# Performance work log

Measured on AMD Instinct MI355X. Metric: run time of the kernel, lower is better.

The kernel has to match this reference:

```python
import jax, jax.numpy as jnp
import numpy as np

NEG_SLOPE = 0.2  # PyG GATConv default negative_slope


def gat_conv(x, W, a_src, a_dst, bias, src, dst, heads, out_c, concat):
    """PyG-style GATConv with self-loops. x:[N,F_in], W:[F_in,heads*out_c]."""
    N = x.shape[0]
    # add self loops
    loop = jnp.arange(N, dtype=src.dtype)
    src = jnp.concatenate([src, loop])
    dst = jnp.concatenate([dst, loop])
    h = (x @ W).reshape(N, heads, out_c)            # [N,H,C]
    alpha_src = jnp.sum(h * a_src, axis=-1)          # [N,H]
    alpha_dst = jnp.sum(h * a_dst, axis=-1)          # [N,H]
    e = jax.nn.leaky_relu(alpha_src[src] + alpha_dst[dst], NEG_SLOPE)  # [E,H]
    # segment softmax over incoming edges of each destination node
    m = jax.ops.segment_max(e, dst, num_segments=N)  # [N,H]
    ex = jnp.exp(e - m[dst])
    s = jax.ops.segment_sum(ex, dst, num_segments=N)
    alpha = ex / (s[dst] + 1e-16)                    # [E,H]
    msg = h[src] * alpha[:, :, None]                 # [E,H,C]
    out = jax.ops.segment_sum(msg, dst, num_segments=N)  # [N,H,C]
    out = out.reshape(N, heads * out_c) if concat else out.mean(axis=1)
    return out + bias


def setup_inputs() -> dict:
    key = jax.random.key(0)
    ks = jax.random.split(key, 16)
    N, E = 25000, 400000
    node_dim, hidden, out_dim, heads = 64, 128, 256, 4

    def glorot(k, shape):
        fan = shape[0] + shape[-1]
        return jax.random.normal(k, shape, jnp.float32) * np.sqrt(2.0 / fan)

    return {
        "x": jax.random.normal(ks[0], (N, node_dim), jnp.float32),
        "edge_index": jax.random.randint(ks[1], (2, E), 0, N, jnp.int32),
        "W_emb": glorot(ks[2], (node_dim, hidden)),
        "b_emb": jnp.zeros((hidden,), jnp.float32),
        "W1": glorot(ks[3], (hidden, heads * hidden)),
        "a1_src": glorot(ks[4], (heads, hidden)),
        "a1_dst": glorot(ks[5], (heads, hidden)),
        "b1": jnp.zeros((heads * hidden,), jnp.float32),
        "W2": glorot(ks[6], (heads * hidden, hidden)),
        "a2_src": glorot(ks[7], (1, hidden)),
        "a2_dst": glorot(ks[8], (1, hidden)),
        "b2": jnp.zeros((hidden,), jnp.float32),
        "W_out": glorot(ks[9], (hidden, out_dim)),
        "b_out": jnp.zeros((out_dim,), jnp.float32),
    }


def reference(x, edge_index, W_emb, b_emb, W1, a1_src, a1_dst, b1, W2, a2_src, a2_dst, b2, W_out, b_out):
    src, dst = edge_index[0], edge_index[1]
    heads, hidden = a1_src.shape[0], a1_src.shape[1]
    h = jax.nn.relu(x @ W_emb + b_emb)                 # dropout is identity in eval
    h = gat_conv(h, W1, a1_src, a1_dst, b1, src, dst, heads, hidden, True)
    h = jax.nn.elu(h)
    h = gat_conv(h, W2, a2_src, a2_dst, b2, src, dst, 1, hidden, False)
    h = jax.nn.elu(h)
    g = jnp.mean(h, axis=0, keepdims=True)             # global mean pool, batch=None -> [1, hidden]
    return g @ W_out + b_out                           # [1, out_dim]
```

## Files before the change

### kernel.cpp

```cpp
#include <hip/hip_runtime.h>
#include <hip/hip_bf16.h>


#define LRELU(x) ((x) > 0.f ? (x) : 0.2f * (x))

typedef short bf16x8 __attribute__((ext_vector_type(8)));
typedef float f32x4 __attribute__((ext_vector_type(4)));
typedef float f32x2 __attribute__((ext_vector_type(2)));

static __device__ __forceinline__ unsigned short f2b(float f) {
    union { float f; unsigned u; } x; x.f = f;
    unsigned r = x.u + 0x7fff + ((x.u >> 16) & 1);
    return (unsigned short)(r >> 16);
}
static __device__ __forceinline__ float rl_f(float v, int c) {
    return __int_as_float(__builtin_amdgcn_readlane(__float_as_int(v), c));
}
static __device__ __forceinline__ unsigned char f2fp8(float v) {
    int p = __builtin_amdgcn_cvt_pk_fp8_f32(v, v, 0, false);
    return (unsigned char)(p & 0xff);
}

__global__ void zero_kernel(int* __restrict__ deg, float* __restrict__ pool,
                            int* __restrict__ done, int* __restrict__ flg,
                            int* __restrict__ agg, int N, int nb) {
    int i = blockIdx.x * blockDim.x + threadIdx.x;
    if (i < N) { deg[i] = 0; return; }
    i -= N;
    if (i < 128) { pool[i] = 0.f; return; }
    i -= 128;
    if (i == 0) { *done = 0; return; }
    i -= 1;
    if (i < nb) { flg[i] = 0; return; }
    i -= nb;
    if (i < nb) agg[i] = 0;
}

__global__ void degcount_prep(const int* __restrict__ ei, int E, int N,
                              int* __restrict__ deg, int blocksE,
                              const float* __restrict__ x, const float* __restrict__ We,
                              const float* __restrict__ W1, const float* __restrict__ W2,
                              unsigned short* __restrict__ xb, unsigned short* __restrict__ WeT,
                              unsigned short* __restrict__ W1T, unsigned short* __restrict__ W2T,
                              int Nx) {
    if ((int)blockIdx.x < blocksE) {
        int i = blockIdx.x * blockDim.x + threadIdx.x;
        if (i < E) atomicAdd(&deg[ei[E + i]], 1);
        else if (i < E + N) atomicAdd(&deg[i - E], 1);
        return;
    }
    int i = (blockIdx.x - blocksE) * blockDim.x + threadIdx.x;
    if (i < Nx) { xb[i] = f2b(x[i]); return; }
    i -= Nx;
    if (i < 64 * 128) { int k = i >> 7, n = i & 127; WeT[n * 64 + k] = f2b(We[i]); return; }
    i -= 64 * 128;
    if (i < 128 * 512) { int k = i >> 9, n = i & 511; W1T[n * 128 + k] = f2b(W1[i]); return; }
    i -= 128 * 512;
    if (i < 512 * 128) { int k = i >> 7, n = i & 127; W2T[n * 512 + k] = f2b(W2[i]); return; }
}

__global__ __launch_bounds__(256) void scan_lookback(const int* __restrict__ deg,
                                                     int* __restrict__ rowptr,
                                                     int* __restrict__ cursor,
                                                     int* __restrict__ agg,
                                                     int* __restrict__ flg,
                                                     int N, int nb) {
    __shared__ int sd[256];
    __shared__ int soff;
    int t = threadIdx.x, b = blockIdx.x;
    int i = b * 256 + t;
    int d = (i < N) ? deg[i] : 0;
    sd[t] = d;
    __syncthreads();
    for (int off = 1; off < 256; off <<= 1) {
        int v = (t >= off) ? sd[t - off] : 0;
        __syncthreads();
        sd[t] += v;
        __syncthreads();
    }
    int incl = sd[t];
    int btot = sd[255];
    if (t == 0) {
        soff = 0;
        __hip_atomic_store(&agg[b], btot, __ATOMIC_RELAXED, __HIP_MEMORY_SCOPE_AGENT);
        __hip_atomic_store(&flg[b], 1, __ATOMIC_RELEASE, __HIP_MEMORY_SCOPE_AGENT);
    }
    if (b > 0 && t < 64) {
        int acc = 0;
        for (int p = t; p < b; p += 64) {
            while (__hip_atomic_load(&flg[p], __ATOMIC_ACQUIRE, __HIP_MEMORY_SCOPE_AGENT) == 0)
                __builtin_amdgcn_s_sleep(1);
            acc += __hip_atomic_load(&agg[p], __ATOMIC_RELAXED, __HIP_MEMORY_SCOPE_AGENT);
        }
#pragma unroll
        for (int o = 32; o >= 1; o >>= 1) acc += __shfl_xor(acc, o);
        if (t == 0) soff = acc;
    }
    __syncthreads();
    int off = soff;
    int excl = off + incl - d;
    if (i < N) { rowptr[i] = excl; cursor[i] = excl; }
    if (b == nb - 1 && t == 255) rowptr[N] = off + btot;
}

__global__ __launch_bounds__(256) void scatter_gemm12(const int* __restrict__ ei, int E, int Nn,
                                                      int* __restrict__ cursor, int* __restrict__ esrc,
                                                      int blocksE,
                                                      const unsigned short* __restrict__ A,
                                                      const unsigned short* __restrict__ WeT,
                                                      const float* __restrict__ b_emb,
                                                      const unsigned short* __restrict__ W1T,
                                                      unsigned char* __restrict__ C8,
                                                      const float* __restrict__ a_src,
                                                      const float* __restrict__ a_dst,
                                                      float* __restrict__ as_out,
                                                      float* __restrict__ ad_out, int M) {
    __shared__ __align__(16) unsigned short smem[22016];
    __shared__ float sAl[128][2];

    if ((int)blockIdx.x < blocksE) {
        int i = blockIdx.x * 256 + threadIdx.x;
        int s, d;
        if (i < E) { s = ei[i]; d = ei[E + i]; }
        else if (i < E + Nn) { s = i - E; d = s; }
        else return;
        int pos = atomicAdd(&cursor[d], 1);
        esrc[pos] = s;
        return;
    }

    unsigned short* Asx = smem;
    unsigned short* Bwe = smem + 9216;
    unsigned short* h0s = smem;
    unsigned short* Bs  = smem + 16896;

    int g = blockIdx.x - blocksE;
    int bx = g & 3, by = g >> 2;
    int tid = threadIdx.x;
    int gm0 = by * 128, gn0 = bx * 128;
    int w = tid >> 6, lane = tid & 63;
    int wrow = (w >> 1) * 64, wcol = (w & 1) * 64;
    int l15 = lane & 15, quad = lane >> 4;

    f32x4 acc[4][4];
#pragma unroll
    for (int i = 0; i < 4; i++)
#pragma unroll
        for (int j = 0; j < 4; j++) acc[i][j] = {0.f, 0.f, 0.f, 0.f};

#pragma unroll
    for (int rr = 0; rr < 4; rr++) {
        int lin = tid + rr * 256;
        int row = lin >> 3;
        int cg = (lin & 7) * 8;
        int grow = gm0 + row; if (grow >= M) grow = M - 1;
        *(uint4*)&Asx[row * 72 + cg] = *(const uint4*)&A[(size_t)grow * 64 + cg];
        *(uint4*)&Bwe[row * 72 + cg] = *(const uint4*)&WeT[(size_t)row * 64 + cg];
    }
    __syncthreads();
#pragma unroll
    for (int k0 = 0; k0 < 64; k0 += 32) {
        bf16x8 af[4], bfr[4];
#pragma unroll
        for (int i = 0; i < 4; i++) {
            af[i]  = *(const bf16x8*)&Asx[(wrow + i * 16 + l15) * 72 + k0 + quad * 8];
            bfr[i] = *(const bf16x8*)&Bwe[(wcol + i * 16 + l15) * 72 + k0 + quad * 8];
        }
#pragma unroll
        for (int i = 0; i < 4; i++)
#pragma unroll
            for (int j = 0; j < 4; j++)
                acc[i][j] = __builtin_amdgcn_mfma_f32_16x16x32_bf16(af[i], bfr[j], acc[i][j], 0, 0, 0);
    }
    __syncthreads();

#pragma unroll
    for (int j = 0; j < 4; j++) {
        int col = wcol + j * 16 + l15;
        float bv = b_emb[col];
#pragma unroll
        for (int i = 0; i < 4; i++) {
            int row = wrow + i * 16 + quad * 4;
#pragma unroll
            for (int r = 0; r < 4; r++) {
                float v = fmaxf(acc[i][j][r] + bv, 0.f);
                h0s[(row + r) * 132 + col] = f2b(v);
            }
        }
    }

#pragma unroll
    for (int i = 0; i < 4; i++)
#pragma unroll
        for (int j = 0; j < 4; j++) acc[i][j] = {0.f, 0.f, 0.f, 0.f};

    for (int k0 = 0; k0 < 128; k0 += 32) {
#pragma unroll
        for (int rr = 0; rr < 2; rr++) {
            int lin = tid + rr * 256;
            int row = lin >> 2;
            int cg = (lin & 3) * 8;
            *(uint4*)&Bs[row * 40 + cg] = *(const uint4*)&W1T[(size_t)(gn0 + row) * 128 + k0 + cg];
        }
        __syncthreads();
        bf16x8 af[4], bfr[4];
#pragma unroll
        for (int i = 0; i < 4; i++) {
            af[i]  = *(const bf16x8*)&h0s[(wrow + i * 16 + l15) * 132 + k0 + quad * 8];
            bfr[i] = *(const bf16x8*)&Bs[(wcol + i * 16 + l15) * 40 + quad * 8];
        }
#pragma unroll
        for (int i = 0; i < 4; i++)
#pragma unroll
            for (int j = 0; j < 4; j++)
                acc[i][j] = __builtin_amdgcn_mfma_f32_16x16x32_bf16(af[i], bfr[j], acc[i][j], 0, 0, 0);
        __syncthreads();
    }

#pragma unroll
    for (int i = 0; i < 4; i++) {
        int row = gm0 + wrow + i * 16 + quad * 4;
#pragma unroll
        for (int j = 0; j < 4; j++) {
            int col = gn0 + wcol + j * 16 + l15;
#pragma unroll
            for (int r = 0; r < 4; r++) {
                int gr = row + r;
                if (gr < M) C8[(size_t)gr * 512 + col] = f2fp8(acc[i][j][r]);
            }
        }
    }

    {
        int hh = bx;
        float as_c[4], ad_c[4];
#pragma unroll
        for (int j = 0; j < 4; j++) {
            int c = gn0 + wcol + j * 16 + l15;
            as_c[j] = a_src[c];
            ad_c[j] = a_dst[c];
        }
#pragma unroll
        for (int i = 0; i < 4; i++) {
#pragma unroll
            for (int r = 0; r < 4; r++) {
                float ps = 0.f, pd = 0.f;
#pragma unroll
                for (int j = 0; j < 4; j++) {
                    ps += acc[i][j][r] * as_c[j];
                    pd += acc[i][j][r] * ad_c[j];
                }
#pragma unroll
                for (int o = 1; o < 16; o <<= 1) {
                    ps += __shfl_xor(ps, o);
                    pd += __shfl_xor(pd, o);
                }
                if (wcol == 64 && l15 == 0) {
                    int lr = wrow + i * 16 + quad * 4 + r;
                    sAl[lr][0] = ps;
                    sAl[lr][1] = pd;
                }
            }
        }
        __syncthreads();
        if (wcol == 0) {
#pragma unroll
            for (int i = 0; i < 4; i++) {
#pragma unroll
                for (int r = 0; r < 4; r++) {
                    float ps = 0.f, pd = 0.f;
#pragma unroll
                    for (int j = 0; j < 4; j++) {
                        ps += acc[i][j][r] * as_c[j];
                        pd += acc[i][j][r] * ad_c[j];
                    }
#pragma unroll
                    for (int o = 1; o < 16; o <<= 1) {
                        ps += __shfl_xor(ps, o);
                        pd += __shfl_xor(pd, o);
                    }
                    if (l15 == 0) {
                        int lr = wrow + i * 16 + quad * 4 + r;
                        int gr = gm0 + lr;
                        if (gr < M) {
                            as_out[(size_t)gr * 4 + hh] = ps + sAl[lr][0];
                            ad_out[(size_t)gr * 4 + hh] = pd + sAl[lr][1];
                        }
                    }
                }
            }
        }
    }
}

template <int ACT, int OFMT, int ALPHA, int H>
__global__ __launch_bounds__(256) void gemm_mfma_nt(const unsigned short* __restrict__ A,
                                                    const unsigned short* __restrict__ Bt,
                                                    const float* __restrict__ bias,
                                                    void* __restrict__ Cout,
                                                    const float* __restrict__ a_src,
                                                    const float* __restrict__ a_dst,
                                                    float* __restrict__ as_out,
                                                    float* __restrict__ ad_out,
                                                    int M, int N, int K) {
    __shared__ __align__(16) unsigned short As[128 * 40];
    __shared__ __align__(16) unsigned short Bs[128 * 40];
    __shared__ float sAl[128][2];
    int tid = threadIdx.x;
    int gm0 = blockIdx.y * 128, gn0 = blockIdx.x * 128;
    int w = tid >> 6, lane = tid & 63;
    int wrow = (w >> 1) * 64, wcol = (w & 1) * 64;
    int l15 = lane & 15, quad = lane >> 4;

    f32x4 acc[4][4];
#pragma unroll
    for (int i = 0; i < 4; i++)
#pragma unroll
        for (int j = 0; j < 4; j++) acc[i][j] = {0.f, 0.f, 0.f, 0.f};

    for (int k0 = 0; k0 < K; k0 += 32) {
#pragma unroll
        for (int rr = 0; rr < 2; rr++) {
            int lin = tid + rr * 256;
            int row = lin >> 2;
            int cg = (lin & 3) * 8;
            int grow = gm0 + row; if (grow >= M) grow = M - 1;
            uint4 va = *(const uint4*)&A[(size_t)grow * K + k0 + cg];
            *(uint4*)&As[row * 40 + cg] = va;
            uint4 vb = *(const uint4*)&Bt[(size_t)(gn0 + row) * K + k0 + cg];
            *(uint4*)&Bs[row * 40 + cg] = vb;
        }
        __syncthreads();
        bf16x8 af[4], bfr[4];
#pragma unroll
        for (int i = 0; i < 4; i++) {
            af[i]  = *(const bf16x8*)&As[(wrow + i * 16 + l15) * 40 + quad * 8];
            bfr[i] = *(const bf16x8*)&Bs[(wcol + i * 16 + l15) * 40 + quad * 8];
        }
#pragma unroll
        for (int i = 0; i < 4; i++)
#pragma unroll
            for (int j = 0; j < 4; j++)
                acc[i][j] = __builtin_amdgcn_mfma_f32_16x16x32_bf16(af[i], bfr[j], acc[i][j], 0, 0, 0);
        __syncthreads();
    }

    if (OFMT == 0) {
        unsigned short* C = (unsigned short*)Cout;
#pragma unroll
        for (int i = 0; i < 4; i++) {
            int row = gm0 + wrow + i * 16 + quad * 4;
#pragma unroll
            for (int j = 0; j < 4; j++) {
                int col = gn0 + wcol + j * 16 + l15;
                float bv = bias ? bias[col] : 0.f;
#pragma unroll
                for (int r = 0; r < 4; r++) {
                    int gr = row + r;
                    if (gr < M) {
                        float v = acc[i][j][r] + bv;
                        if (ACT == 1) v = fmaxf(v, 0.f);
                        C[(size_t)gr * N + col] = f2b(v);
                    }
                }
            }
        }
    } else {
        unsigned char* C8 = (unsigned char*)Cout;
#pragma unroll
        for (int i = 0; i < 4; i++) {
            int row = gm0 + wrow + i * 16 + quad * 4;
#pragma unroll
            for (int j = 0; j < 4; j++) {
                int col = gn0 + wcol + j * 16 + l15;
#pragma unroll
                for (int r = 0; r < 4; r++) {
                    int gr = row + r;
                    if (gr < M) C8[(size_t)gr * N + col] = f2fp8(acc[i][j][r]);
                }
            }
        }
    }

    if (ALPHA) {
        int hh = blockIdx.x;
        float as_c[4], ad_c[4];
#pragma unroll
        for (int j = 0; j < 4; j++) {
            int c = gn0 + wcol + j * 16 + l15;
            as_c[j] = a_src[c];
            ad_c[j] = a_dst[c];
        }
#pragma unroll
        for (int i = 0; i < 4; i++) {
#pragma unroll
            for (int r = 0; r < 4; r++) {
                float ps = 0.f, pd = 0.f;
#pragma unroll
                for (int j = 0; j < 4; j++) {
                    ps += acc[i][j][r] * as_c[j];
                    pd += acc[i][j][r] * ad_c[j];
                }
#pragma unroll
                for (int o = 1; o < 16; o <<= 1) {
                    ps += __shfl_xor(ps, o);
                    pd += __shfl_xor(pd, o);
                }
                if (wcol == 64 && l15 == 0) {
                    int lr = wrow + i * 16 + quad * 4 + r;
                    sAl[lr][0] = ps;
                    sAl[lr][1] = pd;
                }
            }
        }
        __syncthreads();
        if (wcol == 0) {
#pragma unroll
            for (int i = 0; i < 4; i++) {
#pragma unroll
                for (int r = 0; r < 4; r++) {
                    float ps = 0.f, pd = 0.f;
#pragma unroll
                    for (int j = 0; j < 4; j++) {
                        ps += acc[i][j][r] * as_c[j];
                        pd += acc[i][j][r] * ad_c[j];
                    }
#pragma unroll
                    for (int o = 1; o < 16; o <<= 1) {
                        ps += __shfl_xor(ps, o);
                        pd += __shfl_xor(pd, o);
                    }
                    if (l15 == 0) {
                        int lr = wrow + i * 16 + quad * 4 + r;
                        int gr = gm0 + lr;
                        if (gr < M) {
                            as_out[(size_t)gr * H + hh] = ps + sAl[lr][0];
                            ad_out[(size_t)gr * H + hh] = pd + sAl[lr][1];
                        }
                    }
                }
            }
        }
    }
}

__global__ __launch_bounds__(256) void gat_agg_l1(const unsigned* __restrict__ hq,
                                                  const float4* __restrict__ as4,
                                                  const float4* __restrict__ ad4,
                                                  const int* __restrict__ rowptr,
                                                  const int* __restrict__ esrc,
                                                  const float* __restrict__ bias,
                                                  unsigned short* __restrict__ out, int N) {
    __shared__ float wlds_all[4][256];
    int w = threadIdx.x >> 6, lane = threadIdx.x & 63;
    int n = blockIdx.x * 4 + w;
    if (n >= N) return;
    float* wlds = wlds_all[w];
    int2 rp = *(const int2*)&rowptr[n];
    int begin = rp.x, deg = rp.y - rp.x;
    float4 adn = ad4[n];

    int s_l0 = 0;
    float4 e0 = {-3.4e38f, -3.4e38f, -3.4e38f, -3.4e38f};
    if (lane < deg) {
        s_l0 = esrc[begin + lane];
        float4 u = as4[s_l0];
        e0.x = LRELU(u.x + adn.x); e0.y = LRELU(u.y + adn.y);
        e0.z = LRELU(u.z + adn.z); e0.w = LRELU(u.w + adn.w);
    }
    float4 m = e0;
    for (int base = 64; base < deg; base += 64) {
        int j = base + lane;
        if (j < deg) {
            float4 u = as4[esrc[begin + j]];
            m.x = fmaxf(m.x, LRELU(u.x + adn.x)); m.y = fmaxf(m.y, LRELU(u.y + adn.y));
            m.z = fmaxf(m.z, LRELU(u.z + adn.z)); m.w = fmaxf(m.w, LRELU(u.w + adn.w));
        }
    }
#pragma unroll
    for (int o = 32; o >= 1; o >>= 1) {
        m.x = fmaxf(m.x, __shfl_xor(m.x, o));
        m.y = fmaxf(m.y, __shfl_xor(m.y, o));
        m.z = fmaxf(m.z, __shfl_xor(m.z, o));
        m.w = fmaxf(m.w, __shfl_xor(m.w, o));
    }
    float4 s4 = {0.f, 0.f, 0.f, 0.f};
    if (lane < deg) {
        s4.x = __expf(e0.x - m.x); s4.y = __expf(e0.y - m.y);
        s4.z = __expf(e0.z - m.z); s4.w = __expf(e0.w - m.w);
    }
    for (int base = 64; base < deg; base += 64) {
        int j = base + lane;
        if (j < deg) {
            float4 u = as4[esrc[begin + j]];
            s4.x += __expf(LRELU(u.x + adn.x) - m.x); s4.y += __expf(LRELU(u.y + adn.y) - m.y);
            s4.z += __expf(LRELU(u.z + adn.z) - m.z); s4.w += __expf(LRELU(u.w + adn.w) - m.w);
        }
    }
#pragma unroll
    for (int o = 32; o >= 1; o >>= 1) {
        s4.x += __shfl_xor(s4.x, o); s4.y += __shfl_xor(s4.y, o);
        s4.z += __shfl_xor(s4.z, o); s4.w += __shfl_xor(s4.w, o);
    }
    float4 inv = {1.f / (s4.x + 1e-16f), 1.f / (s4.y + 1e-16f),
                  1.f / (s4.z + 1e-16f), 1.f / (s4.w + 1e-16f)};

    float acc[8] = {};
    int h = lane >> 4;
#define ACC_E1(q, wgt) { \
    f32x2 p0 = __builtin_amdgcn_cvt_pk_f32_fp8((int)q.x, false); \
    f32x2 p1 = __builtin_amdgcn_cvt_pk_f32_fp8((int)q.x, true);  \
    f32x2 p2 = __builtin_amdgcn_cvt_pk_f32_fp8((int)q.y, false); \
    f32x2 p3 = __builtin_amdgcn_cvt_pk_f32_fp8((int)q.y, true);  \
    acc[0] += wgt * p0.x; acc[1] += wgt * p0.y; acc[2] += wgt * p1.x; acc[3] += wgt * p1.y; \
    acc[4] += wgt * p2.x; acc[5] += wgt * p2.y; acc[6] += wgt * p3.x; acc[7] += wgt * p3.y; }

    for (int base = 0; base < deg; base += 64) {
        int j = base + lane;
        int len = min(64, deg - base);
        int s_l = s_l0;
        float4 e = e0;
        if (base > 0 && j < deg) {
            s_l = esrc[begin + j];
            float4 u = as4[s_l];
            e.x = LRELU(u.x + adn.x); e.y = LRELU(u.y + adn.y);
            e.z = LRELU(u.z + adn.z); e.w = LRELU(u.w + adn.w);
        }
        if (j < deg) {
            float4 wv4 = {__expf(e.x - m.x) * inv.x, __expf(e.y - m.y) * inv.y,
                          __expf(e.z - m.z) * inv.z, __expf(e.w - m.w) * inv.w};
            *(float4*)&wlds[lane * 4] = wv4;
        }
        int c = 0;
        for (; c + 4 <= len; c += 4) {
            int s0 = __builtin_amdgcn_readlane(s_l, c);
            int s1 = __builtin_amdgcn_readlane(s_l, c + 1);
            int s2 = __builtin_amdgcn_readlane(s_l, c + 2);
            int s3 = __builtin_amdgcn_readlane(s_l, c + 3);
            uint2 q0 = *((const uint2*)(hq + (size_t)s0 * 128) + lane);
            uint2 q1 = *((const uint2*)(hq + (size_t)s1 * 128) + lane);
            uint2 q2 = *((const uint2*)(hq + (size_t)s2 * 128) + lane);
            uint2 q3 = *((const uint2*)(hq + (size_t)s3 * 128) + lane);
            float w0 = wlds[c * 4 + h];
            float w1 = wlds[c * 4 + 4 + h];
            float w2 = wlds[c * 4 + 8 + h];
            float w3 = wlds[c * 4 + 12 + h];
            ACC_E1(q0, w0); ACC_E1(q1, w1); ACC_E1(q2, w2); ACC_E1(q3, w3);
        }
        for (; c < len; c++) {
            int s0 = __builtin_amdgcn_readlane(s_l, c);
            uint2 q0 = *((const uint2*)(hq + (size_t)s0 * 128) + lane);
            float w0 = wlds[c * 4 + h];
            ACC_E1(q0, w0);
        }
    }
#undef ACC_E1
    int f0 = lane * 8;
    unsigned pk[4];
#pragma unroll
    for (int k = 0; k < 4; k++) {
        float v0 = acc[2 * k] + bias[f0 + 2 * k];
        float v1 = acc[2 * k + 1] + bias[f0 + 2 * k + 1];
        v0 = v0 > 0.f ? v0 : (__expf(v0) - 1.f);
        v1 = v1 > 0.f ? v1 : (__expf(v1) - 1.f);
        pk[k] = (unsigned)f2b(v0) | ((unsigned)f2b(v1) << 16);
    }
    uint4 pv = {pk[0], pk[1], pk[2], pk[3]};
    *((uint4*)(out + (size_t)n * 512) + lane) = pv;
}

__global__ __launch_bounds__(256) void gat_agg_l2(const unsigned char* __restrict__ hq,
                                                  const float* __restrict__ as,
                                                  const float* __restrict__ ad,
                                                  const int* __restrict__ rowptr,
                                                  const int* __restrict__ esrc,
                                                  const float* __restrict__ bias,
                                                  float* __restrict__ out, int N) {
    int w = threadIdx.x >> 6, lane = threadIdx.x & 63;
    int n = blockIdx.x * 4 + w;
    if (n >= N) return;
    int2 rp = *(const int2*)&rowptr[n];
    int begin = rp.x, deg = rp.y - rp.x;
    float adn = ad[n];

    int s_l0 = 0;
    float e0 = -3.4e38f;
    if (lane < deg) {
        s_l0 = esrc[begin + lane];
        e0 = LRELU(as[s_l0] + adn);
    }
    float m = e0;
    for (int base = 64; base < deg; base += 64) {
        int j = base + lane;
        if (j < deg) m = fmaxf(m, LRELU(as[esrc[begin + j]] + adn));
    }
#pragma unroll
    for (int o = 32; o >= 1; o >>= 1) m = fmaxf(m, __shfl_xor(m, o));

    float s = (lane < deg) ? __expf(e0 - m) : 0.f;
    for (int base = 64; base < deg; base += 64) {
        int j = base + lane;
        if (j < deg) s += __expf(LRELU(as[esrc[begin + j]] + adn) - m);
    }
#pragma unroll
    for (int o = 32; o >= 1; o >>= 1) s += __shfl_xor(s, o);
    float inv = 1.f / (s + 1e-16f);

    float acc0 = 0.f, acc1 = 0.f;
    for (int base = 0; base < deg; base += 64) {
        int j = base + lane;
        int len = min(64, deg - base);
        int s_l = s_l0;
        float e = e0;
        if (base > 0 && j < deg) {
            s_l = esrc[begin + j];
            e = LRELU(as[s_l] + adn);
        }
        float w_l = (j < deg) ? __expf(e - m) * inv : 0.f;
        int c = 0;
        for (; c + 4 <= len; c += 4) {
            int sp0 = __builtin_amdgcn_readlane(s_l, c);
            int sp1 = __builtin_amdgcn_readlane(s_l, c + 1);
            int sp2 = __builtin_amdgcn_readlane(s_l, c + 2);
            int sp3 = __builtin_amdgcn_readlane(s_l, c + 3);
            unsigned short u0 = *((const unsigned short*)(hq + (size_t)sp0 * 128) + lane);
            unsigned short u1 = *((const unsigned short*)(hq + (size_t)sp1 * 128) + lane);
            unsigned short u2 = *((const unsigned short*)(hq + (size_t)sp2 * 128) + lane);
            unsigned short u3 = *((const unsigned short*)(hq + (size_t)sp3 * 128) + lane);
            float w0 = rl_f(w_l, c), w1 = rl_f(w_l, c + 1);
            float w2 = rl_f(w_l, c + 2), w3 = rl_f(w_l, c + 3);
            f32x2 p0 = __builtin_amdgcn_cvt_pk_f32_fp8((int)u0, false);
            f32x2 p1 = __builtin_amdgcn_cvt_pk_f32_fp8((int)u1, false);
            f32x2 p2 = __builtin_amdgcn_cvt_pk_f32_fp8((int)u2, false);
            f32x2 p3 = __builtin_amdgcn_cvt_pk_f32_fp8((int)u3, false);
            acc0 += w0 * p0.x; acc1 += w0 * p0.y;
            acc0 += w1 * p1.x; acc1 += w1 * p1.y;
            acc0 += w2 * p2.x; acc1 += w2 * p2.y;
            acc0 += w3 * p3.x; acc1 += w3 * p3.y;
        }
        for (; c < len; c++) {
            int sp0 = __builtin_amdgcn_readlane(s_l, c);
            float w0 = rl_f(w_l, c);
            unsigned short u0 = *((const unsigned short*)(hq + (size_t)sp0 * 128) + lane);
            f32x2 p0 = __builtin_amdgcn_cvt_pk_f32_fp8((int)u0, false);
            acc0 += w0 * p0.x; acc1 += w0 * p0.y;
        }
    }
    float v0 = acc0 + bias[lane * 2];
    float v1 = acc1 + bias[lane * 2 + 1];
    v0 = v0 > 0.f ? v0 : (__expf(v0) - 1.f);
    v1 = v1 > 0.f ? v1 : (__expf(v1) - 1.f);
    float2 pv = {v0, v1};
    *(float2*)&out[(size_t)n * 128 + lane * 2] = pv;
}

__global__ __launch_bounds__(256) void pool_final_kernel(const float* __restrict__ o2,
                                                         float* __restrict__ pool,
                                                         int* __restrict__ done,
                                                         const float* __restrict__ Wout,
                                                         const float* __restrict__ bout,
                                                         float* __restrict__ out,
                                                         int N, int nblocks, float invN) {
    __shared__ float4 sred[256];
    int f4 = threadIdx.x & 31;
    int r = blockIdx.x * 256 + (threadIdx.x >> 5);
    float4 acc = {0.f, 0.f, 0.f, 0.f};
    for (int i = 0; i < 32; i++, r += 8) {
        if (r < N) {
            float4 v = *(const float4*)&o2[(size_t)r * 128 + f4 * 4];
            acc.x += v.x; acc.y += v.y; acc.z += v.z; acc.w += v.w;
        }
    }
    sred[threadIdx.x] = acc;
    __syncthreads();
    if (threadIdx.x < 32) {
        float4 t = sred[threadIdx.x];
#pragma unroll
        for (int k = 1; k < 8; k++) {
            float4 u = sred[threadIdx.x + 32 * k];
            t.x += u.x; t.y += u.y; t.z += u.z; t.w += u.w;
        }
        atomicAdd(&pool[f4 * 4 + 0], t.x);
        atomicAdd(&pool[f4 * 4 + 1], t.y);
        atomicAdd(&pool[f4 * 4 + 2], t.z);
        atomicAdd(&pool[f4 * 4 + 3], t.w);
    }
    __threadfence();
    __shared__ int isLast;
    if (threadIdx.x == 0) isLast = (atomicAdd(done, 1) == nblocks - 1);
    __syncthreads();
    if (isLast) {
        __shared__ float spool[128];
        if (threadIdx.x < 128) spool[threadIdx.x] = atomicAdd(&pool[threadIdx.x], 0.f);
        __syncthreads();
        int o = threadIdx.x;
        float a = 0.f;
        for (int k = 0; k < 128; k++) a += spool[k] * Wout[k * 256 + o];
        out[o] = a * invN + bout[o];
    }
}

extern "C" void kernel_launch(void* const* d_in, const int* in_sizes, int n_in,
                              void* d_out, int out_size, void* d_ws, size_t ws_size,
                              hipStream_t stream) {
    const float* x      = (const float*)d_in[0];
    const int*   ei     = (const int*)d_in[1];
    const float* W_emb  = (const float*)d_in[2];
    const float* b_emb  = (const float*)d_in[3];
    const float* W1     = (const float*)d_in[4];
    const float* a1_src = (const float*)d_in[5];
    const float* a1_dst = (const float*)d_in[6];
    const float* b1     = (const float*)d_in[7];
    const float* W2     = (const float*)d_in[8];
    const float* a2_src = (const float*)d_in[9];
    const float* a2_dst = (const float*)d_in[10];
    const float* b2     = (const float*)d_in[11];
    const float* W_out  = (const float*)d_in[12];
    const float* b_out  = (const float*)d_in[13];
    float* out = (float*)d_out;

    const int N = in_sizes[0] / 64;
    const int E = in_sizes[1] / 2;
    const int Etot = E + N;
    const int nb = (N + 255) / 256;

    char* ws = (char*)d_ws;
    size_t off = 0;
    auto alloc = [&](size_t bytes) -> void* {
        void* p = ws + off;
        off = (off + bytes + 255) & ~(size_t)255;
        return p;
    };
    typedef unsigned short u16;
    u16* xb    = (u16*)alloc((size_t)N * 64 * 2);
    u16* WeT   = (u16*)alloc((size_t)128 * 64 * 2);
    u16* W1T   = (u16*)alloc((size_t)512 * 128 * 2);
    u16* W2T   = (u16*)alloc((size_t)128 * 512 * 2);
    unsigned char* h1q = (unsigned char*)alloc((size_t)N * 512);
    u16* o1b   = (u16*)alloc((size_t)N * 512 * 2);
    unsigned char* h2q = (unsigned char*)alloc((size_t)N * 128);
    float* o2  = (float*)alloc((size_t)N * 128 * 4);
    float* as1 = (float*)alloc((size_t)N * 4 * 4);
    float* ad1 = (float*)alloc((size_t)N * 4 * 4);
    float* as2 = (float*)alloc((size_t)N * 4);
    float* ad2 = (float*)alloc((size_t)N * 4);
    float* pool = (float*)alloc(128 * 4);
    int* done   = (int*)alloc(256);
    int* rowptr = (int*)alloc((size_t)(N + 1) * 4);
    int* deg    = (int*)alloc((size_t)N * 4);
    int* cursor = (int*)alloc((size_t)N * 4);
    int* sagg   = (int*)alloc((size_t)nb * 4);
    int* sflg   = (int*)alloc((size_t)nb * 4);
    int* esrc   = (int*)alloc((size_t)Etot * 4);

    const int blocksE = (Etot + 255) / 256;
    const int Nx = N * 64;
    const int prepElems = Nx + 64 * 128 + 128 * 512 + 512 * 128;
    const int prepBlocks = (prepElems + 255) / 256;
    const int mtiles = (N + 127) / 128;
    const int gemmBlocks = 4 * mtiles;

    int zn = N + 128 + 1 + 2 * nb;
    zero_kernel<<<(zn + 255) / 256, 256, 0, stream>>>(deg, pool, done, sflg, sagg, N, nb);

    degcount_prep<<<blocksE + prepBlocks, 256, 0, stream>>>(ei, E, N, deg, blocksE,
                                                            x, W_emb, W1, W2,
                                                            xb, WeT, W1T, W2T, Nx);

    scan_lookback<<<nb, 256, 0, stream>>>(deg, rowptr, cursor, sagg, sflg, N, nb);

    scatter_gemm12<<<blocksE + gemmBlocks, 256, 0, stream>>>(ei, E, N, cursor, esrc, blocksE,
                                                             xb, WeT, b_emb, W1T, h1q,
                                                             a1_src, a1_dst, as1, ad1, N);

    gat_agg_l1<<<(N + 3) / 4, 256, 0, stream>>>((const unsigned*)h1q, (const float4*)as1,
                                                (const float4*)ad1, rowptr, esrc, b1, o1b, N);

    gemm_mfma_nt<0, 1, 1, 1><<<dim3(1, mtiles), 256, 0, stream>>>(
        o1b, W2T, nullptr, h2q, a2_src, a2_dst, as2, ad2, N, 128, 512);

    gat_agg_l2<<<(N + 3) / 4, 256, 0, stream>>>(h2q, as2, ad2, rowptr, esrc, b2, o2, N);

    int npb = (N + 255) / 256;
    pool_final_kernel<<<npb, 256, 0, stream>>>(o2, pool, done, W_out, b_out, out,
                                               N, npb, 1.f / (float)N);
}
```

Measured before the change: 273.4 us.

## Pre-swizzle x and weights into MFMA fragment layout and split scatter from GEMM

The prep kernel now writes x, W_emb and W1 in bf16 in a layout blocked by MFMA fragment, so the fused GEMM loads its A and B operands straight from global memory. This removes the LDS staging and most of the barriers. The edge scatter, which was fused into the GEMM launch, now runs as its own kernel, and the GEMM uses a 2D grid. The trade-off is an extra kernel launch and the loss of overlap between scatter and GEMM. The GEMM also gives up LDS reuse of the B operand across waves, so it relies on the cache instead.

```diff
diff --git a/kernel.cpp b/kernel.cpp
--- a/kernel.cpp
+++ b/kernel.cpp
@@ -40,8 +40,8 @@
                               int* __restrict__ deg, int blocksE,
                               const float* __restrict__ x, const float* __restrict__ We,
                               const float* __restrict__ W1, const float* __restrict__ W2,
-                              unsigned short* __restrict__ xb, unsigned short* __restrict__ WeT,
-                              unsigned short* __restrict__ W1T, unsigned short* __restrict__ W2T,
+                              unsigned short* __restrict__ xbS, unsigned short* __restrict__ WeS,
+                              unsigned short* __restrict__ W1S, unsigned short* __restrict__ W2T,
                               int Nx) {
     if ((int)blockIdx.x < blocksE) {
         int i = blockIdx.x * blockDim.x + threadIdx.x;
@@ -50,11 +50,23 @@
         return;
     }
     int i = (blockIdx.x - blocksE) * blockDim.x + threadIdx.x;
-    if (i < Nx) { xb[i] = f2b(x[i]); return; }
+    if (i < Nx) {
+        int r = i >> 6, k = i & 63;
+        xbS[(r >> 4) * 1024 + (k >> 3) * 128 + (r & 15) * 8 + (k & 7)] = f2b(x[i]);
+        return;
+    }
     i -= Nx;
-    if (i < 64 * 128) { int k = i >> 7, n = i & 127; WeT[n * 64 + k] = f2b(We[i]); return; }
+    if (i < 64 * 128) {
+        int k = i >> 7, n = i & 127;
+        WeS[(n >> 4) * 1024 + (k >> 5) * 512 + ((k >> 3) & 3) * 128 + (n & 15) * 8 + (k & 7)] = f2b(We[i]);
+        return;
+    }
     i -= 64 * 128;
-    if (i < 128 * 512) { int k = i >> 9, n = i & 511; W1T[n * 128 + k] = f2b(W1[i]); return; }
+    if (i < 128 * 512) {
+        int k = i >> 9, n = i & 511;
+        W1S[(n >> 4) * 2048 + (k >> 5) * 512 + ((k >> 3) & 3) * 128 + (n & 15) * 8 + (k & 7)] = f2b(W1[i]);
+        return;
+    }
     i -= 128 * 512;
     if (i < 512 * 128) { int k = i >> 7, n = i & 127; W2T[n * 512 + k] = f2b(W2[i]); return; }
 }
@@ -103,43 +115,34 @@
     if (b == nb - 1 && t == 255) rowptr[N] = off + btot;
 }
 
-__global__ __launch_bounds__(256) void scatter_gemm12(const int* __restrict__ ei, int E, int Nn,
-                                                      int* __restrict__ cursor, int* __restrict__ esrc,
-                                                      int blocksE,
-                                                      const unsigned short* __restrict__ A,
-                                                      const unsigned short* __restrict__ WeT,
-                                                      const float* __restrict__ b_emb,
-                                                      const unsigned short* __restrict__ W1T,
-                                                      unsigned char* __restrict__ C8,
-                                                      const float* __restrict__ a_src,
-                                                      const float* __restrict__ a_dst,
-                                                      float* __restrict__ as_out,
-                                                      float* __restrict__ ad_out, int M) {
-    __shared__ __align__(16) unsigned short smem[22016];
+__global__ void scatter_kernel(const int* __restrict__ ei, int E, int N,
+                               int* __restrict__ cursor, int* __restrict__ esrc) {
+    int i = blockIdx.x * blockDim.x + threadIdx.x;
+    int s, d;
+    if (i < E) { s = ei[i]; d = ei[E + i]; }
+    else if (i < E + N) { s = i - E; d = s; }
+    else return;
+    int pos = atomicAdd(&cursor[d], 1);
+    esrc[pos] = s;
+}
+
+__global__ __launch_bounds__(256) void gemm12_fused(const unsigned short* __restrict__ xbS,
+                                                    const unsigned short* __restrict__ WeS,
+                                                    const float* __restrict__ b_emb,
+                                                    const unsigned short* __restrict__ W1S,
+                                                    unsigned char* __restrict__ C8,
+                                                    const float* __restrict__ a_src,
+                                                    const float* __restrict__ a_dst,
+                                                    float* __restrict__ as_out,
+                                                    float* __restrict__ ad_out, int M) {
+    __shared__ __align__(16) unsigned short h0s[128 * 132];
     __shared__ float sAl[128][2];
 
-    if ((int)blockIdx.x < blocksE) {
-        int i = blockIdx.x * 256 + threadIdx.x;
-        int s, d;
-        if (i < E) { s = ei[i]; d = ei[E + i]; }
-        else if (i < E + Nn) { s = i - E; d = s; }
-        else return;
-        int pos = atomicAdd(&cursor[d], 1);
-        esrc[pos] = s;
-        return;
-    }
-
-    unsigned short* Asx = smem;
-    unsigned short* Bwe = smem + 9216;
-    unsigned short* h0s = smem;
-    unsigned short* Bs  = smem + 16896;
-
-    int g = blockIdx.x - blocksE;
-    int bx = g & 3, by = g >> 2;
     int tid = threadIdx.x;
+    int bx = blockIdx.x, by = blockIdx.y;
     int gm0 = by * 128, gn0 = bx * 128;
     int w = tid >> 6, lane = tid & 63;
-    int wrow = (w >> 1) * 64, wcol = (w & 1) * 64;
+    int wrow = (w >> 1) * 64, wc = w & 1, wcol = wc * 64;
     int l15 = lane & 15, quad = lane >> 4;
 
     f32x4 acc[4][4];
@@ -148,31 +151,21 @@
 #pragma unroll
         for (int j = 0; j < 4; j++) acc[i][j] = {0.f, 0.f, 0.f, 0.f};
 
-#pragma unroll
-    for (int rr = 0; rr < 4; rr++) {
-        int lin = tid + rr * 256;
-        int row = lin >> 3;
-        int cg = (lin & 7) * 8;
-        int grow = gm0 + row; if (grow >= M) grow = M - 1;
-        *(uint4*)&Asx[row * 72 + cg] = *(const uint4*)&A[(size_t)grow * 64 + cg];
-        *(uint4*)&Bwe[row * 72 + cg] = *(const uint4*)&WeT[(size_t)row * 64 + cg];
-    }
-    __syncthreads();
-#pragma unroll
-    for (int k0 = 0; k0 < 64; k0 += 32) {
+    const unsigned short* xA = xbS + (size_t)((gm0 + wrow) >> 4) * 1024 + quad * 128 + l15 * 8;
+    const unsigned short* wB = WeS + (size_t)(wc * 4) * 1024 + quad * 128 + l15 * 8;
+#pragma unroll
+    for (int ks = 0; ks < 2; ks++) {
         bf16x8 af[4], bfr[4];
 #pragma unroll
-        for (int i = 0; i < 4; i++) {
-            af[i]  = *(const bf16x8*)&Asx[(wrow + i * 16 + l15) * 72 + k0 + quad * 8];
-            bfr[i] = *(const bf16x8*)&Bwe[(wcol + i * 16 + l15) * 72 + k0 + quad * 8];
-        }
+        for (int i = 0; i < 4; i++) af[i] = *(const bf16x8*)(xA + i * 1024 + ks * 512);
+#pragma unroll
+        for (int j = 0; j < 4; j++) bfr[j] = *(const bf16x8*)(wB + j * 1024 + ks * 512);
 #pragma unroll
         for (int i = 0; i < 4; i++)
 #pragma unroll
             for (int j = 0; j < 4; j++)
                 acc[i][j] = __builtin_amdgcn_mfma_f32_16x16x32_bf16(af[i], bfr[j], acc[i][j], 0, 0, 0);
     }
-    __syncthreads();
 
 #pragma unroll
     for (int j = 0; j < 4; j++) {
@@ -188,33 +181,26 @@
             }
         }
     }
-
 #pragma unroll
     for (int i = 0; i < 4; i++)
 #pragma unroll
         for (int j = 0; j < 4; j++) acc[i][j] = {0.f, 0.f, 0.f, 0.f};
-
-    for (int k0 = 0; k0 < 128; k0 += 32) {
-#pragma unroll
-        for (int rr = 0; rr < 2; rr++) {
-            int lin = tid + rr * 256;
-            int row = lin >> 2;
-            int cg = (lin & 3) * 8;
-            *(uint4*)&Bs[row * 40 + cg] = *(const uint4*)&W1T[(size_t)(gn0 + row) * 128 + k0 + cg];
-        }
-        __syncthreads();
+    __syncthreads();
+
+    const unsigned short* w1B = W1S + (size_t)(bx * 8 + wc * 4) * 2048 + quad * 128 + l15 * 8;
+#pragma unroll
+    for (int ks = 0; ks < 4; ks++) {
         bf16x8 af[4], bfr[4];
 #pragma unroll
-        for (int i = 0; i < 4; i++) {
-            af[i]  = *(const bf16x8*)&h0s[(wrow + i * 16 + l15) * 132 + k0 + quad * 8];
-            bfr[i] = *(const bf16x8*)&Bs[(wcol + i * 16 + l15) * 40 + quad * 8];
-        }
+        for (int i = 0; i < 4; i++)
+            af[i] = *(const bf16x8*)&h0s[(wrow + i * 16 + l15) * 132 + ks * 32 + quad * 8];
+#pragma unroll
+        for (int j = 0; j < 4; j++) bfr[j] = *(const bf16x8*)(w1B + j * 2048 + ks * 512);
 #pragma unroll
         for (int i = 0; i < 4; i++)
 #pragma unroll
             for (int j = 0; j < 4; j++)
                 acc[i][j] = __builtin_amdgcn_mfma_f32_16x16x32_bf16(af[i], bfr[j], acc[i][j], 0, 0, 0);
-        __syncthreads();
     }
 
 #pragma unroll
@@ -723,6 +709,8 @@
     const int E = in_sizes[1] / 2;
     const int Etot = E + N;
     const int nb = (N + 255) / 256;
+    const int mtiles = (N + 127) / 128;
+    const int nrb = mtiles * 8;
 
     char* ws = (char*)d_ws;
     size_t off = 0;
@@ -732,9 +720,9 @@
         return p;
     };
     typedef unsigned short u16;
-    u16* xb    = (u16*)alloc((size_t)N * 64 * 2);
-    u16* WeT   = (u16*)alloc((size_t)128 * 64 * 2);
-    u16* W1T   = (u16*)alloc((size_t)512 * 128 * 2);
+    u16* xbS   = (u16*)alloc((size_t)nrb * 1024 * 2);
+    u16* WeS   = (u16*)alloc((size_t)8 * 1024 * 2);
+    u16* W1S   = (u16*)alloc((size_t)32 * 2048 * 2);
     u16* W2T   = (u16*)alloc((size_t)128 * 512 * 2);
     unsigned char* h1q = (unsigned char*)alloc((size_t)N * 512);
     u16* o1b   = (u16*)alloc((size_t)N * 512 * 2);
@@ -757,21 +745,20 @@
     const int Nx = N * 64;
     const int prepElems = Nx + 64 * 128 + 128 * 512 + 512 * 128;
     const int prepBlocks = (prepElems + 255) / 256;
-    const int mtiles = (N + 127) / 128;
-    const int gemmBlocks = 4 * mtiles;
 
     int zn = N + 128 + 1 + 2 * nb;
     zero_kernel<<<(zn + 255) / 256, 256, 0, stream>>>(deg, pool, done, sflg, sagg, N, nb);
 
     degcount_prep<<<blocksE + prepBlocks, 256, 0, stream>>>(ei, E, N, deg, blocksE,
                                                             x, W_emb, W1, W2,
-                                                            xb, WeT, W1T, W2T, Nx);
+                                                            xbS, WeS, W1S, W2T, Nx);
 
     scan_lookback<<<nb, 256, 0, stream>>>(deg, rowptr, cursor, sagg, sflg, N, nb);
 
-    scatter_gemm12<<<blocksE + gemmBlocks, 256, 0, stream>>>(ei, E, N, cursor, esrc, blocksE,
-                                                             xb, WeT, b_emb, W1T, h1q,
-                                                             a1_src, a1_dst, as1, ad1, N);
+    scatter_kernel<<<blocksE, 256, 0, stream>>>(ei, E, N, cursor, esrc);
+
+    gemm12_fused<<<dim3(4, mtiles), 256, 0, stream>>>(xbS, WeS, b_emb, W1S, h1q,
+                                                      a1_src, a1_dst, as1, ad1, N);
 
     gat_agg_l1<<<(N + 3) / 4, 256, 0, stream>>>((const unsigned*)h1q, (const float4*)as1,
                                                 (const float4*)ad1, rowptr, esrc, b1, o1b, N);
```

New measurement: 268.6 us. Within noise of the previous version (-1.8%).
